# Performance work log

Measured on AMD Instinct MI355X. Metric: run time of the kernel, lower is better.

The kernel has to match this reference:

```python
import jax, jax.numpy as jnp
import numpy as np

N_HEAD = 8
D_MODEL = 512
D_K = 512
D_V = 512
D_KH = D_K // N_HEAD
D_VH = D_V // N_HEAD
EPS = 1e-6


def setup_inputs() -> dict:
    key = jax.random.key(0)
    ks = jax.random.split(key, 10)
    B, L = 16, 1024
    q = jax.random.normal(ks[0], (B, L, D_MODEL), dtype=jnp.float32)
    k = jax.random.normal(ks[1], (B, L, D_MODEL), dtype=jnp.float32)
    v = jax.random.normal(ks[2], (B, L, D_MODEL), dtype=jnp.float32)
    mask = jax.random.randint(ks[3], (B, L, L), 0, 2).astype(bool)
    s = 1.0 / np.sqrt(D_MODEL)
    Wq = jax.random.normal(ks[4], (D_MODEL, D_K), dtype=jnp.float32) * s
    Wk = jax.random.normal(ks[5], (D_MODEL, D_K), dtype=jnp.float32) * s
    Wv = jax.random.normal(ks[6], (D_MODEL, D_V), dtype=jnp.float32) * s
    Wfc = jax.random.normal(ks[7], (D_V, D_MODEL), dtype=jnp.float32) * (1.0 / np.sqrt(D_V))
    gamma = jnp.ones((D_MODEL,), dtype=jnp.float32)
    beta = jnp.zeros((D_MODEL,), dtype=jnp.float32)
    return {"q": q, "k": k, "v": v, "mask": mask, "Wq": Wq, "Wk": Wk,
            "Wv": Wv, "Wfc": Wfc, "gamma": gamma, "beta": beta}


def reference(q, k, v, mask, Wq, Wk, Wv, Wfc, gamma, beta):
    B, Lq, _ = q.shape
    Lk = k.shape[1]
    residual = q
    # projections -> [B, H, L, d_head]
    qh = (q @ Wq).reshape(B, Lq, N_HEAD, D_KH).transpose(0, 2, 1, 3)
    kh = (k @ Wk).reshape(B, Lk, N_HEAD, D_KH).transpose(0, 2, 1, 3)
    vh = (v @ Wv).reshape(B, Lk, N_HEAD, D_VH).transpose(0, 2, 1, 3)
    # scaled dot-product attention; scale uses per-head dim (source rebinds d_k)
    scores = jnp.einsum('bhqd,bhkd->bhqk', qh / np.sqrt(D_KH), kh)
    scores = jnp.where(mask[:, None, :, :], -1e9, scores)
    attn = jax.nn.softmax(scores, axis=-1)
    out = jnp.einsum('bhqk,bhkd->bhqd', attn, vh)
    out = out.transpose(0, 2, 1, 3).reshape(B, Lq, D_V)
    out = out @ Wfc + residual
    # layer norm
    mu = jnp.mean(out, axis=-1, keepdims=True)
    var = jnp.var(out, axis=-1, keepdims=True)
    out = (out - mu) * jax.lax.rsqrt(var + EPS) * gamma + beta
    return out, attn
```

## Files before the change

### kernel.cpp

```cpp
#include <hip/hip_runtime.h>
#include <hip/hip_bf16.h>

typedef __attribute__((ext_vector_type(8))) short s8v;
typedef __attribute__((ext_vector_type(4))) short s4v;
typedef __attribute__((ext_vector_type(4))) float f4v;

__device__ __forceinline__ short f2bf(float f){
  unsigned u = __builtin_bit_cast(unsigned, f);
  u += 0x7fffu + ((u >> 16) & 1u);
  return (short)(u >> 16);
}

__device__ __forceinline__ f4v mfma16(s8v a, s8v b, f4v c){
  return __builtin_amdgcn_mfma_f32_16x16x32_bf16(a, b, c, 0, 0, 0);
}

__device__ __forceinline__ void ldsbar(){
  asm volatile("s_waitcnt lgkmcnt(0)" ::: "memory");
  __builtin_amdgcn_s_barrier();
  __builtin_amdgcn_sched_barrier(0);
}

#define LOG2E 1.44269504088896f

__global__ __launch_bounds__(256) void prep_kernel(
    const int* __restrict__ mask, unsigned* __restrict__ bits,
    const float* __restrict__ Wq, const float* __restrict__ Wk,
    const float* __restrict__ Wv, const float* __restrict__ Wfc,
    short* __restrict__ Wt)
{
  __shared__ float tile[64][65];
  if (blockIdx.x < 2048){
    const int lane = threadIdx.x & 63;
    const int wid = blockIdx.x*4 + (threadIdx.x >> 6);
    for (int i = 0; i < 32; ++i){
      const int c = wid*32 + i;
      int mv = __builtin_nontemporal_load(&mask[(size_t)c*64 + lane]);
      unsigned long long bal = __ballot(mv != 0);
      if (lane == 0)  bits[c*2]   = (unsigned)bal;
      if (lane == 32) bits[c*2+1] = (unsigned)(bal >> 32);
    }
  } else {
    const int bid = blockIdx.x - 2048;
    const int w = bid >> 6;
    const int tr = (bid & 63) >> 3, tc = bid & 7;
    const int kr0 = tr*64, nc0 = tc*64;
    const float* __restrict__ W = (w==0)?Wq:(w==1)?Wk:(w==2)?Wv:Wfc;
    const int tid = threadIdx.x;
    const int rr = tid >> 6, cc = tid & 63;
    #pragma unroll
    for (int i = 0; i < 16; ++i)
      tile[rr + i*4][cc] = W[(size_t)(kr0 + rr + i*4)*512 + nc0 + cc];
    __syncthreads();
    const int nl = tid >> 2, kc = tid & 3;
    short* dst = Wt + w*262144 + (size_t)(nc0 + nl)*512 + kr0 + kc*16;
    #pragma unroll
    for (int h = 0; h < 2; ++h){
      s8v o;
      #pragma unroll
      for (int j = 0; j < 8; ++j) o[j] = f2bf(tile[kc*16 + h*8 + j][nl]);
      *(s8v*)(dst + h*8) = o;
    }
  }
}

__global__ __launch_bounds__(256) void proj_kernel(
    const float* __restrict__ qin, const float* __restrict__ kin,
    const float* __restrict__ vin, const short* __restrict__ Wt,
    short* __restrict__ Qh, short* __restrict__ Kh, short* __restrict__ Vt)
{
  const int work = (blockIdx.x & 7)*384 + (blockIdx.x >> 3);
  const int z = work >> 10;
  const int r = work & 1023;
  const int mt = r >> 2, nt = r & 3;
  const float* __restrict__ A = (z==0) ? qin : (z==1) ? kin : vin;
  const short* __restrict__ W = Wt + z*262144;
  const int m0 = mt*64, n0 = nt*128;
  __shared__ __align__(16) short Alds[2][64*40];
  __shared__ __align__(16) short Tlds[128*68];
  const int tid = threadIdx.x, lane = tid & 63, wave = tid >> 6;
  const int wm = wave >> 1, wn = wave & 1;
  const int col = lane & 15, kg = lane >> 4;
  f4v acc[2][4];
  #pragma unroll
  for (int i=0;i<2;i++)
    #pragma unroll
    for (int j=0;j<4;j++) acc[i][j] = (f4v){0.f,0.f,0.f,0.f};

  const int arow = tid >> 2, aoff = (tid & 3)*8;
  const float* Ap = A + (size_t)(m0 + arow)*512 + aoff;

  float4 x0 = *(const float4*)(Ap);
  float4 x1 = *(const float4*)(Ap + 4);
  int buf = 0;

  for (int k0 = 0; k0 < 512; k0 += 32){
    s8v ab;
    ab[0]=f2bf(x0.x); ab[1]=f2bf(x0.y); ab[2]=f2bf(x0.z); ab[3]=f2bf(x0.w);
    ab[4]=f2bf(x1.x); ab[5]=f2bf(x1.y); ab[6]=f2bf(x1.z); ab[7]=f2bf(x1.w);
    *(s8v*)&Alds[buf][arow*40 + aoff] = ab;
    if (k0 < 480){
      x0 = *(const float4*)(Ap + k0 + 32);
      x1 = *(const float4*)(Ap + k0 + 36);
    }
    ldsbar();
    s8v af0 = *(const s8v*)&Alds[buf][(wm*32 + col)*40 + kg*8];
    s8v af1 = *(const s8v*)&Alds[buf][(wm*32 + 16 + col)*40 + kg*8];
    #pragma unroll
    for (int f=0; f<4; f++){
      const int n = n0 + wn*64 + f*16 + col;
      s8v bf = *(const s8v*)(W + n*512 + k0 + kg*8);
      acc[0][f] = mfma16(af0, bf, acc[0][f]);
      acc[1][f] = mfma16(af1, bf, acc[1][f]);
    }
    buf ^= 1;
  }

  if (z < 2){
    const float scale = (z==0) ? 0.125f*LOG2E : 1.0f;
    short* D = (z==0) ? Qh : Kh;
    #pragma unroll
    for (int fr=0; fr<2; fr++)
      #pragma unroll
      for (int f=0; f<4; f++)
        #pragma unroll
        for (int j=0; j<4; j++){
          int rr = m0 + wm*32 + fr*16 + kg*4 + j;
          int c = n0 + wn*64 + f*16 + col;
          int b = rr >> 10, l = rr & 1023, hh = c >> 6, d = c & 63;
          D[((size_t)(b*8+hh)*1024 + l)*64 + d] = f2bf(acc[fr][f][j] * scale);
        }
  } else {
    #pragma unroll
    for (int fr=0; fr<2; fr++)
      #pragma unroll
      for (int f=0; f<4; f++)
        #pragma unroll
        for (int j=0; j<4; j++){
          const int rl = wm*32 + fr*16 + kg*4 + j;
          const int cl = wn*64 + f*16 + col;
          Tlds[cl*68 + rl] = f2bf(acc[fr][f][j]);
        }
    ldsbar();
    const int b = m0 >> 10, lbase = m0 & 1023;
    #pragma unroll
    for (int it=0; it<4; ++it){
      const int idx = it*256 + tid;
      const int cl = idx >> 3, rc = idx & 7;
      const int c = n0 + cl, hh = c >> 6, d = c & 63;
      s8v vv = *(const s8v*)&Tlds[cl*68 + rc*8];
      *(s8v*)(Vt + ((size_t)(b*8+hh)*64 + d)*1024 + lbase + rc*8) = vv;
    }
  }
}

__global__ __launch_bounds__(256) void attn_kernel(
  const short* __restrict__ Qh, const short* __restrict__ Kh,
  const short* __restrict__ Vt, const unsigned* __restrict__ bits,
  float* __restrict__ attn, short* __restrict__ ctx)
{
  const int work = ((blockIdx.x & 7) << 8) | (blockIdx.x >> 3);
  const int bh = work >> 4;
  const int q0 = (work & 15) * 64;
  const int b = bh >> 3, h = bh & 7;
  __shared__ unsigned mb[64*33];
  __shared__ __align__(16) short Pb[2][64*128];
  __shared__ float red[256];
  __shared__ float rowinv[64];
  const int tid = threadIdx.x, lane = tid & 63, wave = tid >> 6;
  const int col = lane & 15, kg = lane >> 4;
  const short* Qb = Qh + (size_t)bh*65536;
  const short* Kb = Kh + (size_t)bh*65536;
  const short* Vb = Vt + (size_t)bh*65536;
  const f4v zf = (f4v){0.f,0.f,0.f,0.f};

  {
    const int r = tid >> 2, w = (tid & 3)*8;
    const unsigned* src = bits + (size_t)(b*1024 + q0 + r)*32 + w;
    uint4 w0 = *(const uint4*)src;
    uint4 w1 = *(const uint4*)(src + 4);
    unsigned* dst = &mb[r*33 + w];
    dst[0]=w0.x; dst[1]=w0.y; dst[2]=w0.z; dst[3]=w0.w;
    dst[4]=w1.x; dst[5]=w1.y; dst[6]=w1.z; dst[7]=w1.w;
  }

  s8v qf[4][2];
  #pragma unroll
  for (int qi = 0; qi < 4; ++qi)
    #pragma unroll
    for (int ks = 0; ks < 2; ++ks)
      qf[qi][ks] = *(const s8v*)(Qb + (q0 + qi*16 + col)*64 + ks*32 + kg*8);

  __syncthreads();

  float sum[4] = {0.f, 0.f, 0.f, 0.f};
  f4v cacc[4] = {zf, zf, zf, zf};
  const int d0 = wave*16;
  const int sw = (col & 7) << 3;
  for (int it = 0; it < 8; ++it){
    const int cur = it & 1;
    const int c0 = it*128 + wave*32;
    unsigned mw[4];
    #pragma unroll
    for (int qi = 0; qi < 4; ++qi) mw[qi] = mb[(qi*16 + col)*33 + (c0>>5)];
    #pragma unroll
    for (int ch = 0; ch < 2; ++ch){
      const int cc = c0 + ch*16;
      const short* kp = Kb + (cc + col)*64 + kg*8;
      s8v kf0 = *(const s8v*)kp;
      s8v kf1 = *(const s8v*)(kp + 32);
      #pragma unroll
      for (int qi = 0; qi < 4; ++qi){
        f4v a = mfma16(kf0, qf[qi][0], zf);
        a = mfma16(kf1, qf[qi][1], a);
        s4v pk;
        #pragma unroll
        for (int j = 0; j < 4; ++j){
          const int bit = ch*16 + kg*4 + j;
          float e = exp2f(a[j]);
          float p = ((mw[qi]>>bit)&1) ? 0.f : e;
          sum[qi] += p;
          pk[j] = f2bf(p);
        }
        *(s4v*)&Pb[cur][(qi*16 + col)*128 + ((wave*32 + ch*16 + kg*4) ^ sw)] = pk;
      }
    }
    ldsbar();
    #pragma unroll
    for (int sub = 0; sub < 4; ++sub){
      s8v vf = *(const s8v*)(Vb + (size_t)(d0 + col)*1024 + it*128 + sub*32 + kg*8);
      const int kr = (sub*32 + kg*8) ^ sw;
      #pragma unroll
      for (int qi = 0; qi < 4; ++qi){
        s8v pa = *(const s8v*)&Pb[cur][(qi*16 + col)*128 + kr];
        cacc[qi] = mfma16(pa, vf, cacc[qi]);
      }
    }
  }

  #pragma unroll
  for (int qi = 0; qi < 4; ++qi){
    sum[qi] += __shfl_xor(sum[qi], 16);
    sum[qi] += __shfl_xor(sum[qi], 32);
  }
  if (kg == 0){
    #pragma unroll
    for (int qi = 0; qi < 4; ++qi) red[wave*64 + qi*16 + col] = sum[qi];
  }
  __syncthreads();
  if (tid < 64)
    rowinv[tid] = 1.0f / (red[tid] + red[64+tid] + red[128+tid] + red[192+tid]);
  __syncthreads();

  short* cb = ctx + (size_t)(b*1024 + q0)*512 + h*64 + d0 + col;
  #pragma unroll
  for (int qi = 0; qi < 4; ++qi)
    #pragma unroll
    for (int j = 0; j < 4; ++j)
      cb[(size_t)(qi*16 + kg*4 + j)*512] =
          f2bf(cacc[qi][j] * rowinv[qi*16 + kg*4 + j]);

  float inv[4];
  #pragma unroll
  for (int qi = 0; qi < 4; ++qi) inv[qi] = rowinv[qi*16 + col];
  float* ab = attn + (size_t)(bh*1024 + q0)*1024;
  for (int it = 0; it < 8; ++it){
    const int c0 = it*128 + wave*32;
    unsigned mw[4];
    #pragma unroll
    for (int qi = 0; qi < 4; ++qi) mw[qi] = mb[(qi*16 + col)*33 + (c0>>5)];
    #pragma unroll
    for (int ch = 0; ch < 2; ++ch){
      const int cc = c0 + ch*16;
      const short* kp = Kb + (cc + col)*64 + kg*8;
      s8v kf0 = *(const s8v*)kp;
      s8v kf1 = *(const s8v*)(kp + 32);
      #pragma unroll
      for (int qi = 0; qi < 4; ++qi){
        f4v a = mfma16(kf0, qf[qi][0], zf);
        a = mfma16(kf1, qf[qi][1], a);
        f4v p;
        #pragma unroll
        for (int j = 0; j < 4; ++j){
          const int bit = ch*16 + kg*4 + j;
          float e = exp2f(a[j]) * inv[qi];
          p[j] = ((mw[qi]>>bit)&1) ? 0.f : e;
        }
        __builtin_nontemporal_store(p,
            (f4v*)(ab + (size_t)(qi*16 + col)*1024 + cc + kg*4));
      }
    }
  }
}

__global__ __launch_bounds__(256) void outproj_ln_kernel(
  const short* __restrict__ ctx, const short* __restrict__ Wf,
  const float* __restrict__ resid, const float* __restrict__ gamma,
  const float* __restrict__ beta, float* __restrict__ out)
{
  const int m0 = blockIdx.x * 32;
  __shared__ __align__(16) short Alds[2][32*40];
  __shared__ float sred[32*4], qred[32*4];
  __shared__ float mLds[32], rLds[32];
  const int tid = threadIdx.x, lane = tid & 63, wave = tid >> 6;
  const int col = lane & 15, kg = lane >> 4;
  const int n0 = wave * 128;

  f4v acc[2][8];
  #pragma unroll
  for (int mf=0; mf<2; mf++)
    #pragma unroll
    for (int nf=0; nf<8; nf++) acc[mf][nf] = (f4v){0.f,0.f,0.f,0.f};

  const int arow = tid >> 3, ac = (tid & 7)*4;
  const short* Ap = ctx + (size_t)(m0 + arow)*512 + ac;

  s4v av = *(const s4v*)(Ap);
  int buf = 0;

  for (int k0 = 0; k0 < 512; k0 += 32){
    *(s4v*)&Alds[buf][arow*40 + ac] = av;
    if (k0 < 480) av = *(const s4v*)(Ap + k0 + 32);
    ldsbar();
    s8v af[2];
    #pragma unroll
    for (int mf=0; mf<2; mf++)
      af[mf] = *(const s8v*)&Alds[buf][(mf*16 + col)*40 + kg*8];
    #pragma unroll
    for (int nf=0; nf<8; nf++){
      s8v bf = *(const s8v*)(Wf + (size_t)(n0 + nf*16 + col)*512 + k0 + kg*8);
      #pragma unroll
      for (int mf=0; mf<2; mf++)
        acc[mf][nf] = mfma16(af[mf], bf, acc[mf][nf]);
    }
    buf ^= 1;
  }

  float g[8], bt[8];
  #pragma unroll
  for (int nf=0; nf<8; nf++){
    g[nf]  = gamma[n0 + nf*16 + col];
    bt[nf] = beta[n0 + nf*16 + col];
  }

  #pragma unroll
  for (int mf=0; mf<2; mf++)
    #pragma unroll
    for (int j=0; j<4; j++){
      const int rl = mf*16 + kg*4 + j;
      const size_t r = (size_t)(m0 + rl);
      float s = 0.f, qq = 0.f;
      #pragma unroll
      for (int nf=0; nf<8; nf++){
        float y = acc[mf][nf][j] + resid[r*512 + n0 + nf*16 + col];
        acc[mf][nf][j] = y;
        s += y; qq += y*y;
      }
      #pragma unroll
      for (int d=1; d<16; d<<=1){ s += __shfl_xor(s, d); qq += __shfl_xor(qq, d); }
      if (col == 0){ sred[rl*4 + wave] = s; qred[rl*4 + wave] = qq; }
    }
  __syncthreads();
  if (tid < 32){
    float S = sred[tid*4] + sred[tid*4+1] + sred[tid*4+2] + sred[tid*4+3];
    float Q = qred[tid*4] + qred[tid*4+1] + qred[tid*4+2] + qred[tid*4+3];
    float mean = S * (1.0f/512.0f);
    float var  = Q * (1.0f/512.0f) - mean*mean;
    mLds[tid] = mean;
    rLds[tid] = rsqrtf(var + 1e-6f);
  }
  __syncthreads();

  #pragma unroll
  for (int mf=0; mf<2; mf++)
    #pragma unroll
    for (int j=0; j<4; j++){
      const int rl = mf*16 + kg*4 + j;
      const size_t r = (size_t)(m0 + rl);
      const float mean = mLds[rl], rs = rLds[rl];
      #pragma unroll
      for (int nf=0; nf<8; nf++)
        out[r*512 + n0 + nf*16 + col] = (acc[mf][nf][j] - mean)*rs*g[nf] + bt[nf];
    }
}

extern "C" void kernel_launch(void* const* d_in, const int* in_sizes, int n_in,
                              void* d_out, int out_size, void* d_ws, size_t ws_size,
                              hipStream_t stream) {
  const float* q    = (const float*)d_in[0];
  const float* k    = (const float*)d_in[1];
  const float* v    = (const float*)d_in[2];
  const int*   mask = (const int*)d_in[3];
  const float* Wq   = (const float*)d_in[4];
  const float* Wk   = (const float*)d_in[5];
  const float* Wv   = (const float*)d_in[6];
  const float* Wfc  = (const float*)d_in[7];
  const float* gamma= (const float*)d_in[8];
  const float* beta = (const float*)d_in[9];

  char* ws = (char*)d_ws;
  short* Wt  = (short*)(ws);
  short* Qh  = (short*)(ws + ((size_t)2<<20));
  short* Kh  = (short*)(ws + ((size_t)18<<20));
  short* Vt  = (short*)(ws + ((size_t)34<<20));
  short* ctx = (short*)(ws + ((size_t)50<<20));

  float* out  = (float*)d_out;
  float* attn = out + (size_t)16384*512;
  unsigned* bits = (unsigned*)d_out;

  prep_kernel<<<dim3(2304,1,1), 256, 0, stream>>>(mask, bits, Wq, Wk, Wv, Wfc, Wt);
  proj_kernel <<<dim3(3072,1,1), 256, 0, stream>>>(q, k, v, Wt, Qh, Kh, Vt);
  attn_kernel <<<dim3(2048,1,1), 256, 0, stream>>>(Qh, Kh, Vt, bits, attn, ctx);
  outproj_ln_kernel<<<dim3(512,1,1), 256, 0, stream>>>(ctx, Wt + 3*262144, q,
                                                       gamma, beta, out);
}
```

Baseline: 332.8 us.

## Split attn-prob write into separate kernel co-scheduled with out-projection LN

The attention kernel now computes only the context and row normalizers, stashing the reciprocal row sums and the mask bits in the attn output buffer. A new fused kernel interleaves blocks that recompute QK^T and write the normalized, masked probabilities with blocks that run the output projection and LayerNorm, so the heavy attn store overlaps with the GEMM work. The cost is recomputing QK^T scores and extra stash traffic through global memory. It also depends on each probability block reading its stash before overwriting that region.

```diff
diff --git a/kernel.cpp b/kernel.cpp
--- a/kernel.cpp
+++ b/kernel.cpp
@@ -154,7 +154,7 @@
   }
 }
 
-__global__ __launch_bounds__(256) void attn_kernel(
+__global__ __launch_bounds__(256) void attn_ctx_kernel(
   const short* __restrict__ Qh, const short* __restrict__ Kh,
   const short* __restrict__ Vt, const unsigned* __restrict__ bits,
   float* __restrict__ attn, short* __restrict__ ctx)
@@ -260,128 +260,170 @@
       cb[(size_t)(qi*16 + kg*4 + j)*512] =
           f2bf(cacc[qi][j] * rowinv[qi*16 + kg*4 + j]);
 
-  float inv[4];
+  float* stash = attn + (size_t)(bh*1024 + q0)*1024;
+  if (tid < 64) stash[tid] = rowinv[tid];
+  unsigned* ustash = (unsigned*)stash;
   #pragma unroll
-  for (int qi = 0; qi < 4; ++qi) inv[qi] = rowinv[qi*16 + col];
-  float* ab = attn + (size_t)(bh*1024 + q0)*1024;
-  for (int it = 0; it < 8; ++it){
-    const int c0 = it*128 + wave*32;
-    unsigned mw[4];
-    #pragma unroll
-    for (int qi = 0; qi < 4; ++qi) mw[qi] = mb[(qi*16 + col)*33 + (c0>>5)];
-    #pragma unroll
-    for (int ch = 0; ch < 2; ++ch){
-      const int cc = c0 + ch*16;
-      const short* kp = Kb + (cc + col)*64 + kg*8;
-      s8v kf0 = *(const s8v*)kp;
-      s8v kf1 = *(const s8v*)(kp + 32);
-      #pragma unroll
-      for (int qi = 0; qi < 4; ++qi){
-        f4v a = mfma16(kf0, qf[qi][0], zf);
-        a = mfma16(kf1, qf[qi][1], a);
-        f4v p;
-        #pragma unroll
-        for (int j = 0; j < 4; ++j){
-          const int bit = ch*16 + kg*4 + j;
-          float e = exp2f(a[j]) * inv[qi];
-          p[j] = ((mw[qi]>>bit)&1) ? 0.f : e;
-        }
-        __builtin_nontemporal_store(p,
-            (f4v*)(ab + (size_t)(qi*16 + col)*1024 + cc + kg*4));
-      }
-    }
-  }
-}
-
-__global__ __launch_bounds__(256) void outproj_ln_kernel(
+  for (int i = 0; i < 8; ++i){
+    const int idx = tid*8 + i;
+    ustash[64 + idx] = mb[(idx>>5)*33 + (idx&31)];
+  }
+}
+
+__global__ __launch_bounds__(256) void fused_kernel(
+  const short* __restrict__ Qh, const short* __restrict__ Kh,
+  float* __restrict__ attn,
   const short* __restrict__ ctx, const short* __restrict__ Wf,
   const float* __restrict__ resid, const float* __restrict__ gamma,
   const float* __restrict__ beta, float* __restrict__ out)
 {
-  const int m0 = blockIdx.x * 32;
+  __shared__ unsigned mb[64*33];
+  __shared__ float rowLds[64];
   __shared__ __align__(16) short Alds[2][32*40];
   __shared__ float sred[32*4], qred[32*4];
   __shared__ float mLds[32], rLds[32];
   const int tid = threadIdx.x, lane = tid & 63, wave = tid >> 6;
   const int col = lane & 15, kg = lane >> 4;
-  const int n0 = wave * 128;
-
-  f4v acc[2][8];
-  #pragma unroll
-  for (int mf=0; mf<2; mf++)
-    #pragma unroll
-    for (int nf=0; nf<8; nf++) acc[mf][nf] = (f4v){0.f,0.f,0.f,0.f};
-
-  const int arow = tid >> 3, ac = (tid & 7)*4;
-  const short* Ap = ctx + (size_t)(m0 + arow)*512 + ac;
-
-  s4v av = *(const s4v*)(Ap);
-  int buf = 0;
-
-  for (int k0 = 0; k0 < 512; k0 += 32){
-    *(s4v*)&Alds[buf][arow*40 + ac] = av;
-    if (k0 < 480) av = *(const s4v*)(Ap + k0 + 32);
-    ldsbar();
-    s8v af[2];
+  const int g = blockIdx.x / 5, slot = blockIdx.x % 5;
+
+  if (slot < 4){
+    const int pb = g*4 + slot;
+    const int work = ((pb & 7) << 8) | (pb >> 3);
+    const int bh = work >> 4;
+    const int q0 = (work & 15) * 64;
+    const short* Qb = Qh + (size_t)bh*65536;
+    const short* Kb = Kh + (size_t)bh*65536;
+    float* ab = attn + (size_t)(bh*1024 + q0)*1024;
+    const f4v zf = (f4v){0.f,0.f,0.f,0.f};
+
+    if (tid < 64) rowLds[tid] = ab[tid];
+    const unsigned* ustash = (const unsigned*)ab;
+    #pragma unroll
+    for (int i = 0; i < 8; ++i){
+      const int idx = tid*8 + i;
+      mb[(idx>>5)*33 + (idx&31)] = ustash[64 + idx];
+    }
+
+    s8v qf[4][2];
+    #pragma unroll
+    for (int qi = 0; qi < 4; ++qi)
+      #pragma unroll
+      for (int ks = 0; ks < 2; ++ks)
+        qf[qi][ks] = *(const s8v*)(Qb + (q0 + qi*16 + col)*64 + ks*32 + kg*8);
+
+    __syncthreads();
+
+    float inv[4];
+    #pragma unroll
+    for (int qi = 0; qi < 4; ++qi) inv[qi] = rowLds[qi*16 + col];
+
+    for (int it = 0; it < 8; ++it){
+      const int c0 = it*128 + wave*32;
+      unsigned mw[4];
+      #pragma unroll
+      for (int qi = 0; qi < 4; ++qi) mw[qi] = mb[(qi*16 + col)*33 + (c0>>5)];
+      #pragma unroll
+      for (int ch = 0; ch < 2; ++ch){
+        const int cc = c0 + ch*16;
+        const short* kp = Kb + (cc + col)*64 + kg*8;
+        s8v kf0 = *(const s8v*)kp;
+        s8v kf1 = *(const s8v*)(kp + 32);
+        #pragma unroll
+        for (int qi = 0; qi < 4; ++qi){
+          f4v a = mfma16(kf0, qf[qi][0], zf);
+          a = mfma16(kf1, qf[qi][1], a);
+          f4v p;
+          #pragma unroll
+          for (int j = 0; j < 4; ++j){
+            const int bit = ch*16 + kg*4 + j;
+            float e = exp2f(a[j]) * inv[qi];
+            p[j] = ((mw[qi]>>bit)&1) ? 0.f : e;
+          }
+          __builtin_nontemporal_store(p,
+              (f4v*)(ab + (size_t)(qi*16 + col)*1024 + cc + kg*4));
+        }
+      }
+    }
+  } else {
+    const int m0 = g * 32;
+    f4v acc[2][8];
     #pragma unroll
     for (int mf=0; mf<2; mf++)
-      af[mf] = *(const s8v*)&Alds[buf][(mf*16 + col)*40 + kg*8];
+      #pragma unroll
+      for (int nf=0; nf<8; nf++) acc[mf][nf] = (f4v){0.f,0.f,0.f,0.f};
+
+    const int n0 = wave * 128;
+    const int arow = tid >> 3, ac = (tid & 7)*4;
+    const short* Ap = ctx + (size_t)(m0 + arow)*512 + ac;
+
+    s4v av = *(const s4v*)(Ap);
+    int buf = 0;
+
+    for (int k0 = 0; k0 < 512; k0 += 32){
+      *(s4v*)&Alds[buf][arow*40 + ac] = av;
+      if (k0 < 480) av = *(const s4v*)(Ap + k0 + 32);
+      ldsbar();
+      s8v af[2];
+      #pragma unroll
+      for (int mf=0; mf<2; mf++)
+        af[mf] = *(const s8v*)&Alds[buf][(mf*16 + col)*40 + kg*8];
+      #pragma unroll
+      for (int nf=0; nf<8; nf++){
+        s8v bf = *(const s8v*)(Wf + (size_t)(n0 + nf*16 + col)*512 + k0 + kg*8);
+        #pragma unroll
+        for (int mf=0; mf<2; mf++)
+          acc[mf][nf] = mfma16(af[mf], bf, acc[mf][nf]);
+      }
+      buf ^= 1;
+    }
+
+    float gm[8], bt[8];
     #pragma unroll
     for (int nf=0; nf<8; nf++){
-      s8v bf = *(const s8v*)(Wf + (size_t)(n0 + nf*16 + col)*512 + k0 + kg*8);
-      #pragma unroll
-      for (int mf=0; mf<2; mf++)
-        acc[mf][nf] = mfma16(af[mf], bf, acc[mf][nf]);
-    }
-    buf ^= 1;
-  }
-
-  float g[8], bt[8];
-  #pragma unroll
-  for (int nf=0; nf<8; nf++){
-    g[nf]  = gamma[n0 + nf*16 + col];
-    bt[nf] = beta[n0 + nf*16 + col];
-  }
-
-  #pragma unroll
-  for (int mf=0; mf<2; mf++)
-    #pragma unroll
-    for (int j=0; j<4; j++){
-      const int rl = mf*16 + kg*4 + j;
-      const size_t r = (size_t)(m0 + rl);
-      float s = 0.f, qq = 0.f;
-      #pragma unroll
-      for (int nf=0; nf<8; nf++){
-        float y = acc[mf][nf][j] + resid[r*512 + n0 + nf*16 + col];
-        acc[mf][nf][j] = y;
-        s += y; qq += y*y;
-      }
-      #pragma unroll
-      for (int d=1; d<16; d<<=1){ s += __shfl_xor(s, d); qq += __shfl_xor(qq, d); }
-      if (col == 0){ sred[rl*4 + wave] = s; qred[rl*4 + wave] = qq; }
-    }
-  __syncthreads();
-  if (tid < 32){
-    float S = sred[tid*4] + sred[tid*4+1] + sred[tid*4+2] + sred[tid*4+3];
-    float Q = qred[tid*4] + qred[tid*4+1] + qred[tid*4+2] + qred[tid*4+3];
-    float mean = S * (1.0f/512.0f);
-    float var  = Q * (1.0f/512.0f) - mean*mean;
-    mLds[tid] = mean;
-    rLds[tid] = rsqrtf(var + 1e-6f);
-  }
-  __syncthreads();
-
-  #pragma unroll
-  for (int mf=0; mf<2; mf++)
-    #pragma unroll
-    for (int j=0; j<4; j++){
-      const int rl = mf*16 + kg*4 + j;
-      const size_t r = (size_t)(m0 + rl);
-      const float mean = mLds[rl], rs = rLds[rl];
-      #pragma unroll
-      for (int nf=0; nf<8; nf++)
-        out[r*512 + n0 + nf*16 + col] = (acc[mf][nf][j] - mean)*rs*g[nf] + bt[nf];
-    }
+      gm[nf] = gamma[n0 + nf*16 + col];
+      bt[nf] = beta[n0 + nf*16 + col];
+    }
+
+    #pragma unroll
+    for (int mf=0; mf<2; mf++)
+      #pragma unroll
+      for (int j=0; j<4; j++){
+        const int rl = mf*16 + kg*4 + j;
+        const size_t r = (size_t)(m0 + rl);
+        float s = 0.f, qq = 0.f;
+        #pragma unroll
+        for (int nf=0; nf<8; nf++){
+          float y = acc[mf][nf][j] + resid[r*512 + n0 + nf*16 + col];
+          acc[mf][nf][j] = y;
+          s += y; qq += y*y;
+        }
+        #pragma unroll
+        for (int d=1; d<16; d<<=1){ s += __shfl_xor(s, d); qq += __shfl_xor(qq, d); }
+        if (col == 0){ sred[rl*4 + wave] = s; qred[rl*4 + wave] = qq; }
+      }
+    __syncthreads();
+    if (tid < 32){
+      float S = sred[tid*4] + sred[tid*4+1] + sred[tid*4+2] + sred[tid*4+3];
+      float Q = qred[tid*4] + qred[tid*4+1] + qred[tid*4+2] + qred[tid*4+3];
+      float mean = S * (1.0f/512.0f);
+      float var  = Q * (1.0f/512.0f) - mean*mean;
+      mLds[tid] = mean;
+      rLds[tid] = rsqrtf(var + 1e-6f);
+    }
+    __syncthreads();
+
+    #pragma unroll
+    for (int mf=0; mf<2; mf++)
+      #pragma unroll
+      for (int j=0; j<4; j++){
+        const int rl = mf*16 + kg*4 + j;
+        const size_t r = (size_t)(m0 + rl);
+        const float mean = mLds[rl], rs = rLds[rl];
+        #pragma unroll
+        for (int nf=0; nf<8; nf++)
+          out[r*512 + n0 + nf*16 + col] = (acc[mf][nf][j] - mean)*rs*gm[nf] + bt[nf];
+      }
+  }
 }
 
 extern "C" void kernel_launch(void* const* d_in, const int* in_sizes, int n_in,
@@ -411,7 +453,8 @@
 
   prep_kernel<<<dim3(2304,1,1), 256, 0, stream>>>(mask, bits, Wq, Wk, Wv, Wfc, Wt);
   proj_kernel <<<dim3(3072,1,1), 256, 0, stream>>>(q, k, v, Wt, Qh, Kh, Vt);
-  attn_kernel <<<dim3(2048,1,1), 256, 0, stream>>>(Qh, Kh, Vt, bits, attn, ctx);
-  outproj_ln_kernel<<<dim3(512,1,1), 256, 0, stream>>>(ctx, Wt + 3*262144, q,
-                                                       gamma, beta, out);
-}
+  attn_ctx_kernel<<<dim3(2048,1,1), 256, 0, stream>>>(Qh, Kh, Vt, bits, attn, ctx);
+  fused_kernel<<<dim3(2560,1,1), 256, 0, stream>>>(Qh, Kh, attn, ctx,
+                                                   Wt + 3*262144, q,
+                                                   gamma, beta, out);
+}
```

Result: slower. 394.9 us (+18.7%).
